# Performance work log

Measured on AMD Instinct MI355X. Metric: run time of the kernel, lower is better.

The kernel has to match this reference:

```python
import jax, jax.numpy as jnp
import numpy as np


def setup_inputs() -> dict:
    key = jax.random.key(0)
    ks = jax.random.split(key, 8)
    NUM_REL, D, E2, NUM_ENT = 500, 128, 3000000, 200000
    return {
        "rel_embed": jax.random.normal(ks[0], (NUM_REL, D), jnp.float32),
        "rel_embed_in": jax.random.normal(ks[1], (NUM_REL, D), jnp.float32),
        "rel_embed_out": jax.random.normal(ks[2], (NUM_REL, D), jnp.float32),
        "w_in": jax.random.normal(ks[3], (D, D), jnp.float32) * (D ** -0.5),
        "w_out": jax.random.normal(ks[4], (D, D), jnp.float32) * (D ** -0.5),
        "bn_gamma": jnp.ones((D,), jnp.float32),
        "bn_beta": jnp.zeros((D,), jnp.float32),
        "edge_index": jax.random.randint(ks[5], (2, E2), 0, NUM_ENT, jnp.int64 if jax.config.x64_enabled else jnp.int32),
        "edge_type": jax.random.randint(ks[6], (E2,), 0, NUM_REL, jnp.int64 if jax.config.x64_enabled else jnp.int32),
        "num_ent": NUM_ENT,
    }


def _edge_norm(edge_index, num_ent):
    # symmetric-normalization: deg^-1/2[row] * deg^-1/2[col]
    row, col = edge_index[0], edge_index[1]
    deg = jax.ops.segment_sum(jnp.ones(row.shape, jnp.float32), row, num_segments=num_ent)
    deg_inv = jnp.where(deg > 0, jax.lax.rsqrt(deg), 0.0)
    return deg_inv[row] * deg_inv[col]


def reference(rel_embed, rel_embed_in, rel_embed_out, w_in, w_out,
              bn_gamma, bn_beta, edge_index, edge_type, num_ent):
    E = edge_index.shape[1] // 2  # first half incoming, second half outgoing
    norm_in = _edge_norm(edge_index[:, :E], num_ent)    # [E]
    norm_out = _edge_norm(edge_index[:, E:], num_ent)   # [E]

    # gather relation embeds per edge, transform (per-edge matmul)
    neighs_in = rel_embed_in[edge_type[:E]] @ w_in      # [E, D]
    neighs_out = rel_embed_out[edge_type[E:]] @ w_out   # [E, D]

    # norm-weighted scatter-sum into entity buckets (rel_agg == 'sum')
    res_in = jax.ops.segment_sum(neighs_in * norm_in[:, None], edge_index[0, :E], num_segments=num_ent)
    res_out = jax.ops.segment_sum(neighs_out * norm_out[:, None], edge_index[0, E:], num_segments=num_ent)

    h = 0.5 * res_in + 0.5 * res_out                    # [num_ent, D]
    # BatchNorm1d (training mode: batch stats, biased variance, eps=1e-5)
    mean = jnp.mean(h, axis=0)
    var = jnp.mean(jnp.square(h - mean), axis=0)
    res = jnp.tanh((h - mean) * jax.lax.rsqrt(var + 1e-5) * bn_gamma + bn_beta)
    return (res, rel_embed)
```

## Files before the change

kernel.cpp:

```cpp
#include <hip/hip_runtime.h>

#define D 128
#define BUNROLL 8
#define RPB 128
#define CAP 2560
#define MAXK 2048
#define CHUNK4 8192
#define STILE 1024

__device__ __forceinline__ unsigned f2bf_rne(float x) {
    unsigned u = __float_as_uint(x);
    return (u + 0x7fffu + ((u >> 16) & 1u)) >> 16;
}

__global__ void transform2_bf_kernel(const float* __restrict__ Rin, const float* __restrict__ Win,
                                     const float* __restrict__ Rout, const float* __restrict__ Wout,
                                     unsigned short* __restrict__ T_bf, int nrel) {
    __shared__ float row[D];
    int b = blockIdx.x;
    bool second = (b >= nrel);
    const float* R = second ? Rout : Rin;
    const float* W = second ? Wout : Win;
    int r = second ? b - nrel : b;
    int t = threadIdx.x;
    row[t] = R[r * D + t];
    __syncthreads();
    float acc = 0.f;
#pragma unroll 8
    for (int k = 0; k < D; ++k) acc += row[k] * W[k * D + t];
    T_bf[(size_t)b * D + t] = (unsigned short)f2bf_rne(acc);
}

__global__ void transform2_kernel(const float* __restrict__ Rin, const float* __restrict__ Win,
                                  const float* __restrict__ Rout, const float* __restrict__ Wout,
                                  float* __restrict__ T_all, int nrel) {
    __shared__ float row[D];
    int b = blockIdx.x;
    bool second = (b >= nrel);
    const float* R = second ? Rout : Rin;
    const float* W = second ? Wout : Win;
    int r = second ? b - nrel : b;
    int t = threadIdx.x;
    row[t] = R[r * D + t];
    __syncthreads();
    float acc = 0.f;
#pragma unroll 8
    for (int k = 0; k < D; ++k) acc += row[k] * W[k * D + t];
    T_all[(size_t)b * D + t] = acc;
}

__global__ __launch_bounds__(512) void hist4_kernel(
        const int* __restrict__ rows, int E2,
        unsigned* __restrict__ cnt, int NB, int K) {
    __shared__ unsigned h[MAXK];
    int tid = threadIdx.x, blk = blockIdx.x;
    for (int i = tid; i < K; i += 512) h[i] = 0;
    __syncthreads();
    long s = (long)blk * CHUNK4;
    long e = s + CHUNK4; if (e > E2) e = E2;
    long n = e - s;
    if ((n & 3) == 0) {
        const int4* r4 = (const int4*)(rows + s);
        int m = (int)(n >> 2);
        for (int i = tid; i < m; i += 512) {
            int4 r = r4[i];
            atomicAdd(&h[((unsigned)r.x) >> 7], 1u);
            atomicAdd(&h[((unsigned)r.y) >> 7], 1u);
            atomicAdd(&h[((unsigned)r.z) >> 7], 1u);
            atomicAdd(&h[((unsigned)r.w) >> 7], 1u);
        }
    } else {
        for (long i = s + tid; i < e; i += 512)
            atomicAdd(&h[((unsigned)rows[i]) >> 7], 1u);
    }
    __syncthreads();
    for (int i = tid; i < K; i += 512)
        cnt[(size_t)i * NB + blk] = h[i];
}

__global__ __launch_bounds__(256) void tile_sum_u32(const unsigned int* __restrict__ cnt,
                                                    unsigned int* __restrict__ tsum, int n) {
    int tid = threadIdx.x;
    int i0 = blockIdx.x * STILE + tid * 4;
    unsigned int s = 0;
#pragma unroll
    for (int k = 0; k < 4; ++k) {
        int i = i0 + k;
        if (i < n) s += cnt[i];
    }
    __shared__ unsigned int ls[256];
    ls[tid] = s;
    __syncthreads();
    for (int off = 128; off >= 1; off >>= 1) {
        if (tid < off) ls[tid] += ls[tid + off];
        __syncthreads();
    }
    if (tid == 0) tsum[blockIdx.x] = ls[0];
}

__global__ void scan_tiles_kernel(const unsigned int* __restrict__ tile_sums,
                                  unsigned int* __restrict__ tile_off,
                                  unsigned int* __restrict__ base, int ntiles, int n) {
    int t = threadIdx.x;
    __shared__ unsigned int ls[1024];
    unsigned int v = (t < ntiles) ? tile_sums[t] : 0u;
    ls[t] = v;
    __syncthreads();
    for (int off = 1; off < 1024; off <<= 1) {
        unsigned int add = (t >= off) ? ls[t - off] : 0u;
        __syncthreads();
        ls[t] += add;
        __syncthreads();
    }
    if (t < ntiles) tile_off[t] = ls[t] - v;
    if (t == 1023) base[n] = ls[1023];
}

__global__ __launch_bounds__(256) void base_write_u32(const unsigned int* __restrict__ cnt,
                                                      const unsigned int* __restrict__ tile_off,
                                                      unsigned int* __restrict__ base, int n) {
    int tid = threadIdx.x;
    int i0 = blockIdx.x * STILE + tid * 4;
    unsigned int c[4];
#pragma unroll
    for (int k = 0; k < 4; ++k) {
        int i = i0 + k;
        c[k] = (i < n) ? cnt[i] : 0u;
    }
    unsigned int s = c[0] + c[1] + c[2] + c[3];
    __shared__ unsigned int ls[256];
    ls[tid] = s;
    __syncthreads();
    for (int off = 1; off < 256; off <<= 1) {
        unsigned int add = (tid >= off) ? ls[tid - off] : 0u;
        __syncthreads();
        ls[tid] += add;
        __syncthreads();
    }
    unsigned int run = (tid > 0 ? ls[tid - 1] : 0u) + tile_off[blockIdx.x];
#pragma unroll
    for (int k = 0; k < 4; ++k) {
        int i = i0 + k;
        if (i < n) base[i] = run;
        run += c[k];
    }
}

__global__ __launch_bounds__(512) void scatter4_kernel(
        const int* __restrict__ rows, const int* __restrict__ cols,
        const int* __restrict__ etype, const unsigned* __restrict__ base,
        uint2* __restrict__ payload, int E, int E2, int nrel, int NB, int K) {
    __shared__ unsigned cur[MAXK];
    int tid = threadIdx.x, blk = blockIdx.x;
    for (int i = tid; i < K; i += 512) cur[i] = base[(size_t)i * NB + blk];
    __syncthreads();
    long s = (long)blk * CHUNK4;
    long e = s + CHUNK4; if (e > E2) e = E2;
    long n = e - s;
    if ((n & 3) == 0) {
        const int4* r4 = (const int4*)(rows + s);
        const int4* c4 = (const int4*)(cols + s);
        const int4* t4 = (const int4*)(etype + s);
        int m = (int)(n >> 2);
        for (int i = tid; i < m; i += 512) {
            int4 r = r4[i];
            int4 c = c4[i];
            int4 t = t4[i];
            long e0 = s + ((long)i << 2);
            unsigned pos, ty;
            ty = (unsigned)t.x + ((e0 + 0 < E) ? 0u : (unsigned)nrel);
            pos = atomicAdd(&cur[((unsigned)r.x) >> 7], 1u);
            payload[pos] = make_uint2((unsigned)c.x, (((unsigned)r.x & 127u) << 10) | ty);
            ty = (unsigned)t.y + ((e0 + 1 < E) ? 0u : (unsigned)nrel);
            pos = atomicAdd(&cur[((unsigned)r.y) >> 7], 1u);
            payload[pos] = make_uint2((unsigned)c.y, (((unsigned)r.y & 127u) << 10) | ty);
            ty = (unsigned)t.z + ((e0 + 2 < E) ? 0u : (unsigned)nrel);
            pos = atomicAdd(&cur[((unsigned)r.z) >> 7], 1u);
            payload[pos] = make_uint2((unsigned)c.z, (((unsigned)r.z & 127u) << 10) | ty);
            ty = (unsigned)t.w + ((e0 + 3 < E) ? 0u : (unsigned)nrel);
            pos = atomicAdd(&cur[((unsigned)r.w) >> 7], 1u);
            payload[pos] = make_uint2((unsigned)c.w, (((unsigned)r.w & 127u) << 10) | ty);
        }
    } else {
        for (long i = s + tid; i < e; i += 512) {
            unsigned r = (unsigned)rows[i];
            unsigned c = (unsigned)cols[i];
            unsigned t = (unsigned)etype[i];
            unsigned ty = t + ((i < E) ? 0u : (unsigned)nrel);
            unsigned pos = atomicAdd(&cur[r >> 7], 1u);
            payload[pos] = make_uint2(c, ((r & 127u) << 10) | ty);
        }
    }
}

__global__ __launch_bounds__(512) void degsort_kernel(
        const unsigned* __restrict__ base, const uint2* __restrict__ payload,
        float* __restrict__ dinvAll, unsigned* __restrict__ rowBase,
        int nent, int nrel, int NB, int K) {
    __shared__ unsigned h2[RPB * 2];
    __shared__ unsigned sc[RPB];
    int tid = threadIdx.x, b = blockIdx.x;
    if (tid < RPB * 2) h2[tid] = 0;
    __syncthreads();
    size_t NBK = (size_t)NB * K;
    unsigned s = base[(size_t)b * NB];
    unsigned e = (b + 1 < K) ? base[(size_t)(b + 1) * NB] : base[NBK];
    for (unsigned i = s + tid; i < e; i += 512) {
        unsigned y = payload[i].y;
        unsigned lr = (y >> 10) & 127u;
        unsigned fo = ((y & 1023u) >= (unsigned)nrel) ? 1u : 0u;
        atomicAdd(&h2[lr * 2 + fo], 1u);
    }
    __syncthreads();
    unsigned tot = 0;
    if (tid < RPB) { tot = h2[tid * 2] + h2[tid * 2 + 1]; sc[tid] = tot; }
    __syncthreads();
    for (int off = 1; off < RPB; off <<= 1) {
        unsigned v = 0;
        if (tid < RPB && tid >= off) v = sc[tid - off];
        __syncthreads();
        if (tid < RPB) sc[tid] += v;
        __syncthreads();
    }
    if (tid < RPB) {
        rowBase[(size_t)b * RPB + tid] = sc[tid] - tot;
        int row = (b << 7) + tid;
        if (row < nent) {
            unsigned a = h2[tid * 2], o = h2[tid * 2 + 1];
            dinvAll[row]        = a ? rsqrtf((float)a) : 0.f;
            dinvAll[nent + row] = o ? rsqrtf((float)o) : 0.f;
        }
    }
}

__global__ __launch_bounds__(512) void accum4_kernel(
        const unsigned* __restrict__ base, const uint2* __restrict__ payload,
        const unsigned short* __restrict__ T_bf, const float* __restrict__ dinvAll,
        const unsigned* __restrict__ rowBase,
        float* __restrict__ out, float* __restrict__ sums, float* __restrict__ sumsq,
        int nent, int nrel, int NB, int K) {
    __shared__ uint2 sp[CAP];
    __shared__ unsigned hstart[RPB];
    __shared__ unsigned hcur[RPB];
    __shared__ float ls[D], lq[D];
    int tid = threadIdx.x;
    int b = blockIdx.x;
    size_t NBK = (size_t)NB * K;
    unsigned start = base[(size_t)b * NB];
    unsigned end   = (b + 1 < K) ? base[(size_t)(b + 1) * NB] : base[NBK];
    int n = (int)(end - start);
    int nin = n < CAP ? n : CAP;

    if (tid < RPB) { ls[tid] = 0.f; lq[tid] = 0.f; }

    if (n <= CAP) {
        if (tid < RPB) {
            unsigned v = rowBase[(size_t)b * RPB + tid];
            hstart[tid] = v;
            hcur[tid] = v;
        }
        __syncthreads();
        for (int i = tid; i < nin; i += 512) {
            uint2 p = payload[start + i];
            unsigned pos = atomicAdd(&hcur[(p.y >> 10) & 127u], 1u);
            sp[pos] = p;
        }
        __syncthreads();
    } else {
        if (tid < RPB) hstart[tid] = 0;
        __syncthreads();
        for (int i = tid; i < nin; i += 512)
            atomicAdd(&hstart[(payload[start + i].y >> 10) & 127u], 1u);
        __syncthreads();
        for (int off = 1; off < RPB; off <<= 1) {
            unsigned v = 0;
            if (tid < RPB && tid >= off) v = hstart[tid - off];
            __syncthreads();
            if (tid < RPB) hstart[tid] += v;
            __syncthreads();
        }
        unsigned ex = 0;
        if (tid < RPB) ex = tid ? hstart[tid - 1] : 0u;
        __syncthreads();
        if (tid < RPB) { hstart[tid] = ex; hcur[tid] = ex; }
        __syncthreads();
        for (int i = tid; i < nin; i += 512) {
            uint2 p = payload[start + i];
            unsigned pos = atomicAdd(&hcur[(p.y >> 10) & 127u], 1u);
            sp[pos] = p;
        }
        __syncthreads();
    }

    const uint2* T2 = (const uint2*)T_bf;
    float4* out4 = (float4*)out;
    int hw = tid >> 5, l32 = tid & 31;
    int row0 = b << 7;
    unsigned unrel = (unsigned)nrel;
    float4 s4 = make_float4(0.f, 0.f, 0.f, 0.f);
    float4 q4 = make_float4(0.f, 0.f, 0.f, 0.f);
    for (int rr = 0; rr < 8; ++rr) {
        int r = (hw << 3) + rr;
        int row = row0 + r;
        float da_in = 0.f, da_out = 0.f;
        if (row < nent) { da_in = dinvAll[row]; da_out = dinvAll[nent + row]; }
        unsigned s0 = hstart[r];
        unsigned s1 = (r < RPB - 1) ? hstart[r + 1] : (unsigned)nin;
        float4 a = make_float4(0.f, 0.f, 0.f, 0.f);
        unsigned i = s0;
        for (; i + 4 <= s1; i += 4) {
            uint2 p0 = sp[i], p1 = sp[i + 1], p2 = sp[i + 2], p3 = sp[i + 3];
            unsigned ty0 = p0.y & 1023u, ty1 = p1.y & 1023u;
            unsigned ty2 = p2.y & 1023u, ty3 = p3.y & 1023u;
            bool f0 = ty0 < unrel, f1 = ty1 < unrel, f2 = ty2 < unrel, f3 = ty3 < unrel;
            float dc0 = dinvAll[(f0 ? 0 : nent) + p0.x];
            float dc1 = dinvAll[(f1 ? 0 : nent) + p1.x];
            float dc2 = dinvAll[(f2 ? 0 : nent) + p2.x];
            float dc3 = dinvAll[(f3 ? 0 : nent) + p3.x];
            uint2 t0 = T2[(size_t)ty0 * 32 + l32];
            uint2 t1 = T2[(size_t)ty1 * 32 + l32];
            uint2 t2 = T2[(size_t)ty2 * 32 + l32];
            uint2 t3 = T2[(size_t)ty3 * 32 + l32];
            float c0 = 0.5f * (f0 ? da_in : da_out) * dc0;
            float c1 = 0.5f * (f1 ? da_in : da_out) * dc1;
            float c2 = 0.5f * (f2 ? da_in : da_out) * dc2;
            float c3 = 0.5f * (f3 ? da_in : da_out) * dc3;
            a.x += c0 * __uint_as_float(t0.x << 16);
            a.y += c0 * __uint_as_float(t0.x & 0xffff0000u);
            a.z += c0 * __uint_as_float(t0.y << 16);
            a.w += c0 * __uint_as_float(t0.y & 0xffff0000u);
            a.x += c1 * __uint_as_float(t1.x << 16);
            a.y += c1 * __uint_as_float(t1.x & 0xffff0000u);
            a.z += c1 * __uint_as_float(t1.y << 16);
            a.w += c1 * __uint_as_float(t1.y & 0xffff0000u);
            a.x += c2 * __uint_as_float(t2.x << 16);
            a.y += c2 * __uint_as_float(t2.x & 0xffff0000u);
            a.z += c2 * __uint_as_float(t2.y << 16);
            a.w += c2 * __uint_as_float(t2.y & 0xffff0000u);
            a.x += c3 * __uint_as_float(t3.x << 16);
            a.y += c3 * __uint_as_float(t3.x & 0xffff0000u);
            a.z += c3 * __uint_as_float(t3.y << 16);
            a.w += c3 * __uint_as_float(t3.y & 0xffff0000u);
        }
        for (; i < s1; ++i) {
            uint2 p = sp[i];
            unsigned ty = p.y & 1023u;
            bool f = ty < unrel;
            float c = 0.5f * (f ? da_in : da_out) * dinvAll[(f ? 0 : nent) + p.x];
            uint2 t = T2[(size_t)ty * 32 + l32];
            a.x += c * __uint_as_float(t.x << 16);
            a.y += c * __uint_as_float(t.x & 0xffff0000u);
            a.z += c * __uint_as_float(t.y << 16);
            a.w += c * __uint_as_float(t.y & 0xffff0000u);
        }
        for (unsigned j = start + (unsigned)nin; j < end; ++j) {
            uint2 p = payload[j];
            if (((p.y >> 10) & 127u) == (unsigned)r) {
                unsigned ty = p.y & 1023u;
                bool f = ty < unrel;
                float c = 0.5f * (f ? da_in : da_out) * dinvAll[(f ? 0 : nent) + p.x];
                uint2 t = T2[(size_t)ty * 32 + l32];
                a.x += c * __uint_as_float(t.x << 16);
                a.y += c * __uint_as_float(t.x & 0xffff0000u);
                a.z += c * __uint_as_float(t.y << 16);
                a.w += c * __uint_as_float(t.y & 0xffff0000u);
            }
        }
        if (row < nent) {
            out4[(size_t)row * 32 + l32] = a;
            s4.x += a.x; s4.y += a.y; s4.z += a.z; s4.w += a.w;
            q4.x += a.x * a.x; q4.y += a.y * a.y; q4.z += a.z * a.z; q4.w += a.w * a.w;
        }
    }
    atomicAdd(&ls[4 * l32 + 0], s4.x); atomicAdd(&ls[4 * l32 + 1], s4.y);
    atomicAdd(&ls[4 * l32 + 2], s4.z); atomicAdd(&ls[4 * l32 + 3], s4.w);
    atomicAdd(&lq[4 * l32 + 0], q4.x); atomicAdd(&lq[4 * l32 + 1], q4.y);
    atomicAdd(&lq[4 * l32 + 2], q4.z); atomicAdd(&lq[4 * l32 + 3], q4.w);
    __syncthreads();
    if (tid < D) {
        atomicAdd(&sums[tid], ls[tid]);
        atomicAdd(&sumsq[tid], lq[tid]);
    }
}

__global__ void bn_coef_kernel(const float* __restrict__ sums, const float* __restrict__ sumsq,
                               const float* __restrict__ gamma, const float* __restrict__ beta,
                               float* __restrict__ scale, float* __restrict__ shift, int nent) {
    int c = threadIdx.x;
    float inv_n = 1.0f / (float)nent;
    float mean = sums[c] * inv_n;
    float var = sumsq[c] * inv_n - mean * mean;
    float istd = rsqrtf(var + 1e-5f);
    float sc = istd * gamma[c];
    scale[c] = sc;
    shift[c] = beta[c] - mean * sc;
}

__global__ __launch_bounds__(256) void bn_apply2_kernel(
        float* __restrict__ h, const float* __restrict__ scale, const float* __restrict__ shift,
        const float* __restrict__ rel_embed, float* __restrict__ pass, int nent, int npass4) {
    __shared__ float s_sc[D], s_sh[D];
    if (threadIdx.x < D) { s_sc[threadIdx.x] = scale[threadIdx.x]; s_sh[threadIdx.x] = shift[threadIdx.x]; }
    __syncthreads();
    long total = (long)nent * (D / 4);
    long stride = (long)gridDim.x * blockDim.x;
    long idx0 = (long)blockIdx.x * blockDim.x + threadIdx.x;
    float4* h4 = (float4*)h;
    for (long i = idx0; i < total; i += stride) {
        int c0 = (int)((i & 31) << 2);
        float4 v = h4[i];
        v.x = tanhf(v.x * s_sc[c0 + 0] + s_sh[c0 + 0]);
        v.y = tanhf(v.y * s_sc[c0 + 1] + s_sh[c0 + 1]);
        v.z = tanhf(v.z * s_sc[c0 + 2] + s_sh[c0 + 2]);
        v.w = tanhf(v.w * s_sc[c0 + 3] + s_sh[c0 + 3]);
        h4[i] = v;
    }
    const float4* re4 = (const float4*)rel_embed;
    float4* p4 = (float4*)pass;
    for (long i = idx0; i < npass4; i += stride) p4[i] = re4[i];
}

__global__ __launch_bounds__(256) void degree_kernel(const int* __restrict__ rows, int E,
                                                     float* __restrict__ deg_in,
                                                     float* __restrict__ deg_out) {
    int total = 2 * E;
    int tid = blockIdx.x * blockDim.x + threadIdx.x;
    int nth = gridDim.x * blockDim.x;
    for (long b = (long)tid * BUNROLL; b < total; b += (long)nth * BUNROLL) {
        for (int k = 0; k < BUNROLL && b + k < total; ++k) {
            int r = rows[b + k];
            float* deg = (b + k < E) ? deg_in : deg_out;
            atomicAdd(&deg[r], 1.0f);
        }
    }
}

__global__ void scatter_kernel(const int* __restrict__ rows, const int* __restrict__ cols,
                               const int* __restrict__ etype,
                               const float* __restrict__ deg_in, const float* __restrict__ deg_out,
                               const float* __restrict__ T_in, const float* __restrict__ T_out,
                               float* __restrict__ out, int E) {
    int wave = (blockIdx.x * blockDim.x + threadIdx.x) >> 6;
    int lane = threadIdx.x & 63;
    int nwaves = (gridDim.x * blockDim.x) >> 6;
    int total = 2 * E;
    for (int e = wave; e < total; e += nwaves) {
        bool first = (e < E);
        int row = rows[e];
        int col = cols[e];
        int t = etype[e];
        const float* deg = first ? deg_in : deg_out;
        const float* T = first ? T_in : T_out;
        float dr = deg[row];
        float dc = deg[col];
        float norm = (dr > 0.f ? rsqrtf(dr) : 0.f) * (dc > 0.f ? rsqrtf(dc) : 0.f);
        float c = 0.5f * norm;
        if (c != 0.f) {
            float v0 = c * T[t * D + lane];
            float v1 = c * T[t * D + 64 + lane];
            long b = (long)row * D;
            atomicAdd(&out[b + lane], v0);
            atomicAdd(&out[b + 64 + lane], v1);
        }
    }
}

__global__ void bn_stats_kernel(const float* __restrict__ h, int nent,
                                float* __restrict__ sums, float* __restrict__ sumsq) {
    int col = threadIdx.x;
    float s = 0.f, s2 = 0.f;
    for (int r = blockIdx.x; r < nent; r += gridDim.x) {
        float v = h[(long)r * D + col];
        s += v;
        s2 += v * v;
    }
    atomicAdd(&sums[col], s);
    atomicAdd(&sumsq[col], s2);
}

__global__ void bn_apply_kernel(float* __restrict__ h,
                                const float* __restrict__ sums, const float* __restrict__ sumsq,
                                const float* __restrict__ gamma, const float* __restrict__ beta,
                                int nent) {
    long total = ((long)nent * D) / 4;
    long stride = (long)gridDim.x * blockDim.x;
    float inv_n = 1.0f / (float)nent;
    float4* h4 = (float4*)h;
    for (long i = (long)blockIdx.x * blockDim.x + threadIdx.x; i < total; i += stride) {
        int c0 = (int)((i * 4) & (D - 1));
        float4 v = h4[i];
        float r[4] = {v.x, v.y, v.z, v.w};
#pragma unroll
        for (int j = 0; j < 4; ++j) {
            int col = c0 + j;
            float mean = sums[col] * inv_n;
            float var = sumsq[col] * inv_n - mean * mean;
            float istd = rsqrtf(var + 1e-5f);
            r[j] = tanhf((r[j] - mean) * istd * gamma[col] + beta[col]);
        }
        h4[i] = make_float4(r[0], r[1], r[2], r[3]);
    }
}

extern "C" void kernel_launch(void* const* d_in, const int* in_sizes, int n_in,
                              void* d_out, int out_size, void* d_ws, size_t ws_size,
                              hipStream_t stream) {
    const float* rel_embed     = (const float*)d_in[0];
    const float* rel_embed_in  = (const float*)d_in[1];
    const float* rel_embed_out = (const float*)d_in[2];
    const float* w_in          = (const float*)d_in[3];
    const float* w_out         = (const float*)d_in[4];
    const float* bn_gamma      = (const float*)d_in[5];
    const float* bn_beta       = (const float*)d_in[6];
    const int*   edge_index    = (const int*)d_in[7];
    const int*   edge_type     = (const int*)d_in[8];

    const int nrel = in_sizes[0] / D;
    const int E2   = in_sizes[8];
    const int E    = E2 / 2;
    const int nent = (out_size - in_sizes[0]) / D;
    const int K    = (nent + RPB - 1) / RPB;
    const int NB   = (E2 + CHUNK4 - 1) / CHUNK4;
    const long NBK = (long)NB * K;
    const int ntiles = (int)((NBK + STILE - 1) / STILE);

    float* out = (float*)d_out;
    const int* rows = edge_index;
    const int* cols = edge_index + E2;

    float*          ws       = (float*)d_ws;
    float*          dinvAll  = ws;
    float*          sums     = dinvAll + (size_t)2 * nent;
    float*          sumsq    = sums + D;
    float*          scale    = sumsq + D;
    float*          shift    = scale + D;
    unsigned*       rowBase  = (unsigned*)(shift + D);
    unsigned*       cnt      = rowBase + (size_t)K * RPB;
    unsigned*       tsum     = cnt + NBK + 1;
    unsigned*       toff     = tsum + ntiles;
    unsigned short* T_bf     = (unsigned short*)(toff + ntiles);
    uintptr_t pal = ((uintptr_t)(T_bf + (size_t)2 * nrel * D) + 15) & ~(uintptr_t)15;
    uint2*          payload  = (uint2*)pal;
    size_t needed = (pal + (size_t)E2 * sizeof(uint2)) - (uintptr_t)d_ws;

    bool fast = (needed <= ws_size) && (K <= MAXK) && (2 * nrel <= 1024) &&
                (ntiles <= 1024);

    if (fast) {
        hipMemsetAsync(sums, 0, (size_t)2 * D * sizeof(float), stream);

        transform2_bf_kernel<<<2 * nrel, D, 0, stream>>>(rel_embed_in, w_in,
                                                         rel_embed_out, w_out, T_bf, nrel);
        hist4_kernel<<<NB, 512, 0, stream>>>(rows, E2, cnt, NB, K);
        tile_sum_u32<<<ntiles, 256, 0, stream>>>(cnt, tsum, (int)NBK);
        scan_tiles_kernel<<<1, 1024, 0, stream>>>(tsum, toff, cnt, ntiles, (int)NBK);
        base_write_u32<<<ntiles, 256, 0, stream>>>(cnt, toff, cnt, (int)NBK);
        scatter4_kernel<<<NB, 512, 0, stream>>>(rows, cols, edge_type, cnt,
                                                payload, E, E2, nrel, NB, K);
        degsort_kernel<<<K, 512, 0, stream>>>(cnt, payload, dinvAll, rowBase,
                                              nent, nrel, NB, K);
        accum4_kernel<<<K, 512, 0, stream>>>(cnt, payload, T_bf, dinvAll, rowBase,
                                             out, sums, sumsq, nent, nrel, NB, K);
        bn_coef_kernel<<<1, D, 0, stream>>>(sums, sumsq, bn_gamma, bn_beta,
                                            scale, shift, nent);
        bn_apply2_kernel<<<2048, 256, 0, stream>>>(out, scale, shift, rel_embed,
                                                   out + (size_t)nent * D, nent,
                                                   (nrel * D) / 4);
    } else {
        float* f_deg_in  = ws;
        float* f_deg_out = f_deg_in + nent;
        float* f_T_in    = f_deg_out + nent;
        float* f_T_out   = f_T_in + (size_t)nrel * D;
        float* f_sums    = f_T_out + (size_t)nrel * D;
        float* f_sumsq   = f_sums + D;

        hipMemsetAsync(out, 0, (size_t)nent * D * sizeof(float), stream);
        hipMemsetAsync(f_deg_in, 0, (size_t)2 * nent * sizeof(float), stream);
        hipMemsetAsync(f_sums, 0, (size_t)2 * D * sizeof(float), stream);

        transform2_kernel<<<2 * nrel, D, 0, stream>>>(rel_embed_in, w_in, rel_embed_out, w_out,
                                                      f_T_in, nrel);
        degree_kernel<<<1466, 256, 0, stream>>>(edge_index, E, f_deg_in, f_deg_out);
        scatter_kernel<<<2048, 256, 0, stream>>>(rows, cols, edge_type, f_deg_in, f_deg_out,
                                                 f_T_in, f_T_out, out, E);
        bn_stats_kernel<<<1024, D, 0, stream>>>(out, nent, f_sums, f_sumsq);
        bn_apply_kernel<<<4096, 256, 0, stream>>>(out, f_sums, f_sumsq, bn_gamma, bn_beta, nent);
        hipMemcpyAsync(out + (size_t)nent * D, rel_embed,
                       (size_t)nrel * D * sizeof(float), hipMemcpyDeviceToDevice, stream);
    }
}
```

Baseline: 227.2 us.

## Store pre-BN activations as bf16 and interleave two rows per warp in accumulation

The accumulation kernel now processes two destination rows at once, interleaving their edge loops to raise memory-level parallelism. It also writes the intermediate h in bf16 to a workspace buffer instead of fp32 into the output, and the BN apply kernel reads that buffer. This halves intermediate write and read traffic (about 100MB down to 50MB each way). The cost is that bf16 rounding of h, applied before normalization, adds precision error. BN statistics are still computed in fp32.

```diff
diff --git a/kernel.cpp b/kernel.cpp
--- a/kernel.cpp
+++ b/kernel.cpp
@@ -12,6 +12,12 @@
     unsigned u = __float_as_uint(x);
     return (u + 0x7fffu + ((u >> 16) & 1u)) >> 16;
 }
+
+#define FMA4(a, c, t)                                        \
+    (a).x += (c) * __uint_as_float((t).x << 16);             \
+    (a).y += (c) * __uint_as_float((t).x & 0xffff0000u);     \
+    (a).z += (c) * __uint_as_float((t).y << 16);             \
+    (a).w += (c) * __uint_as_float((t).y & 0xffff0000u);
 
 __global__ void transform2_bf_kernel(const float* __restrict__ Rin, const float* __restrict__ Win,
                                      const float* __restrict__ Rout, const float* __restrict__ Wout,
@@ -233,11 +239,42 @@
     }
 }
 
+#define DRAIN4(i, s1, a, dain, daout)                                            \
+    for (; (i) + 4 <= (s1); (i) += 4) {                                          \
+        uint2 p0 = sp[(i)], p1 = sp[(i) + 1], p2 = sp[(i) + 2], p3 = sp[(i) + 3];\
+        unsigned ty0 = p0.y & 1023u, ty1 = p1.y & 1023u;                         \
+        unsigned ty2 = p2.y & 1023u, ty3 = p3.y & 1023u;                         \
+        bool f0 = ty0 < unrel, f1 = ty1 < unrel;                                 \
+        bool f2 = ty2 < unrel, f3 = ty3 < unrel;                                 \
+        float dc0 = dinvAll[(f0 ? 0 : nent) + p0.x];                             \
+        float dc1 = dinvAll[(f1 ? 0 : nent) + p1.x];                             \
+        float dc2 = dinvAll[(f2 ? 0 : nent) + p2.x];                             \
+        float dc3 = dinvAll[(f3 ? 0 : nent) + p3.x];                             \
+        uint2 t0 = T2[(size_t)ty0 * 32 + l32];                                   \
+        uint2 t1 = T2[(size_t)ty1 * 32 + l32];                                   \
+        uint2 t2 = T2[(size_t)ty2 * 32 + l32];                                   \
+        uint2 t3 = T2[(size_t)ty3 * 32 + l32];                                   \
+        float c0 = 0.5f * (f0 ? (dain) : (daout)) * dc0;                         \
+        float c1 = 0.5f * (f1 ? (dain) : (daout)) * dc1;                         \
+        float c2 = 0.5f * (f2 ? (dain) : (daout)) * dc2;                         \
+        float c3 = 0.5f * (f3 ? (dain) : (daout)) * dc3;                         \
+        FMA4(a, c0, t0) FMA4(a, c1, t1) FMA4(a, c2, t2) FMA4(a, c3, t3)          \
+    }                                                                            \
+    for (; (i) < (s1); ++(i)) {                                                  \
+        uint2 p = sp[(i)];                                                       \
+        unsigned ty = p.y & 1023u;                                               \
+        bool f = ty < unrel;                                                     \
+        float c = 0.5f * (f ? (dain) : (daout)) * dinvAll[(f ? 0 : nent) + p.x]; \
+        uint2 t = T2[(size_t)ty * 32 + l32];                                     \
+        FMA4(a, c, t)                                                            \
+    }
+
 __global__ __launch_bounds__(512) void accum4_kernel(
         const unsigned* __restrict__ base, const uint2* __restrict__ payload,
         const unsigned short* __restrict__ T_bf, const float* __restrict__ dinvAll,
         const unsigned* __restrict__ rowBase,
-        float* __restrict__ out, float* __restrict__ sums, float* __restrict__ sumsq,
+        float* __restrict__ out, unsigned short* __restrict__ h_bf, int use_bf,
+        float* __restrict__ sums, float* __restrict__ sumsq,
         int nent, int nrel, int NB, int K) {
     __shared__ uint2 sp[CAP];
     __shared__ unsigned hstart[RPB];
@@ -294,82 +331,95 @@
 
     const uint2* T2 = (const uint2*)T_bf;
     float4* out4 = (float4*)out;
+    uint2* hb2 = (uint2*)h_bf;
     int hw = tid >> 5, l32 = tid & 31;
     int row0 = b << 7;
     unsigned unrel = (unsigned)nrel;
     float4 s4 = make_float4(0.f, 0.f, 0.f, 0.f);
     float4 q4 = make_float4(0.f, 0.f, 0.f, 0.f);
-    for (int rr = 0; rr < 8; ++rr) {
-        int r = (hw << 3) + rr;
-        int row = row0 + r;
-        float da_in = 0.f, da_out = 0.f;
-        if (row < nent) { da_in = dinvAll[row]; da_out = dinvAll[nent + row]; }
-        unsigned s0 = hstart[r];
-        unsigned s1 = (r < RPB - 1) ? hstart[r + 1] : (unsigned)nin;
-        float4 a = make_float4(0.f, 0.f, 0.f, 0.f);
-        unsigned i = s0;
-        for (; i + 4 <= s1; i += 4) {
-            uint2 p0 = sp[i], p1 = sp[i + 1], p2 = sp[i + 2], p3 = sp[i + 3];
-            unsigned ty0 = p0.y & 1023u, ty1 = p1.y & 1023u;
-            unsigned ty2 = p2.y & 1023u, ty3 = p3.y & 1023u;
-            bool f0 = ty0 < unrel, f1 = ty1 < unrel, f2 = ty2 < unrel, f3 = ty3 < unrel;
-            float dc0 = dinvAll[(f0 ? 0 : nent) + p0.x];
-            float dc1 = dinvAll[(f1 ? 0 : nent) + p1.x];
-            float dc2 = dinvAll[(f2 ? 0 : nent) + p2.x];
-            float dc3 = dinvAll[(f3 ? 0 : nent) + p3.x];
-            uint2 t0 = T2[(size_t)ty0 * 32 + l32];
-            uint2 t1 = T2[(size_t)ty1 * 32 + l32];
-            uint2 t2 = T2[(size_t)ty2 * 32 + l32];
-            uint2 t3 = T2[(size_t)ty3 * 32 + l32];
-            float c0 = 0.5f * (f0 ? da_in : da_out) * dc0;
-            float c1 = 0.5f * (f1 ? da_in : da_out) * dc1;
-            float c2 = 0.5f * (f2 ? da_in : da_out) * dc2;
-            float c3 = 0.5f * (f3 ? da_in : da_out) * dc3;
-            a.x += c0 * __uint_as_float(t0.x << 16);
-            a.y += c0 * __uint_as_float(t0.x & 0xffff0000u);
-            a.z += c0 * __uint_as_float(t0.y << 16);
-            a.w += c0 * __uint_as_float(t0.y & 0xffff0000u);
-            a.x += c1 * __uint_as_float(t1.x << 16);
-            a.y += c1 * __uint_as_float(t1.x & 0xffff0000u);
-            a.z += c1 * __uint_as_float(t1.y << 16);
-            a.w += c1 * __uint_as_float(t1.y & 0xffff0000u);
-            a.x += c2 * __uint_as_float(t2.x << 16);
-            a.y += c2 * __uint_as_float(t2.x & 0xffff0000u);
-            a.z += c2 * __uint_as_float(t2.y << 16);
-            a.w += c2 * __uint_as_float(t2.y & 0xffff0000u);
-            a.x += c3 * __uint_as_float(t3.x << 16);
-            a.y += c3 * __uint_as_float(t3.x & 0xffff0000u);
-            a.z += c3 * __uint_as_float(t3.y << 16);
-            a.w += c3 * __uint_as_float(t3.y & 0xffff0000u);
-        }
-        for (; i < s1; ++i) {
-            uint2 p = sp[i];
-            unsigned ty = p.y & 1023u;
-            bool f = ty < unrel;
-            float c = 0.5f * (f ? da_in : da_out) * dinvAll[(f ? 0 : nent) + p.x];
-            uint2 t = T2[(size_t)ty * 32 + l32];
-            a.x += c * __uint_as_float(t.x << 16);
-            a.y += c * __uint_as_float(t.x & 0xffff0000u);
-            a.z += c * __uint_as_float(t.y << 16);
-            a.w += c * __uint_as_float(t.y & 0xffff0000u);
-        }
-        for (unsigned j = start + (unsigned)nin; j < end; ++j) {
-            uint2 p = payload[j];
-            if (((p.y >> 10) & 127u) == (unsigned)r) {
-                unsigned ty = p.y & 1023u;
-                bool f = ty < unrel;
-                float c = 0.5f * (f ? da_in : da_out) * dinvAll[(f ? 0 : nent) + p.x];
-                uint2 t = T2[(size_t)ty * 32 + l32];
-                a.x += c * __uint_as_float(t.x << 16);
-                a.y += c * __uint_as_float(t.x & 0xffff0000u);
-                a.z += c * __uint_as_float(t.y << 16);
-                a.w += c * __uint_as_float(t.y & 0xffff0000u);
+
+    for (int rp = 0; rp < 4; ++rp) {
+        int rA = (hw << 3) + rp * 2;
+        int rB = rA + 1;
+        int rowA = row0 + rA, rowB = row0 + rB;
+        float daA_in = 0.f, daA_out = 0.f, daB_in = 0.f, daB_out = 0.f;
+        if (rowA < nent) { daA_in = dinvAll[rowA]; daA_out = dinvAll[nent + rowA]; }
+        if (rowB < nent) { daB_in = dinvAll[rowB]; daB_out = dinvAll[nent + rowB]; }
+        unsigned sA1 = hstart[rA + 1];
+        unsigned sB1 = (rB < RPB - 1) ? hstart[rB + 1] : (unsigned)nin;
+        unsigned iA = hstart[rA], iB = sA1;
+        float4 aA = make_float4(0.f, 0.f, 0.f, 0.f);
+        float4 aB = make_float4(0.f, 0.f, 0.f, 0.f);
+
+        while (iA + 2 <= sA1 && iB + 2 <= sB1) {
+            uint2 pA0 = sp[iA], pA1 = sp[iA + 1];
+            uint2 pB0 = sp[iB], pB1 = sp[iB + 1];
+            unsigned tyA0 = pA0.y & 1023u, tyA1 = pA1.y & 1023u;
+            unsigned tyB0 = pB0.y & 1023u, tyB1 = pB1.y & 1023u;
+            bool fA0 = tyA0 < unrel, fA1 = tyA1 < unrel;
+            bool fB0 = tyB0 < unrel, fB1 = tyB1 < unrel;
+            float dcA0 = dinvAll[(fA0 ? 0 : nent) + pA0.x];
+            float dcA1 = dinvAll[(fA1 ? 0 : nent) + pA1.x];
+            float dcB0 = dinvAll[(fB0 ? 0 : nent) + pB0.x];
+            float dcB1 = dinvAll[(fB1 ? 0 : nent) + pB1.x];
+            uint2 tA0 = T2[(size_t)tyA0 * 32 + l32];
+            uint2 tA1 = T2[(size_t)tyA1 * 32 + l32];
+            uint2 tB0 = T2[(size_t)tyB0 * 32 + l32];
+            uint2 tB1 = T2[(size_t)tyB1 * 32 + l32];
+            float cA0 = 0.5f * (fA0 ? daA_in : daA_out) * dcA0;
+            float cA1 = 0.5f * (fA1 ? daA_in : daA_out) * dcA1;
+            float cB0 = 0.5f * (fB0 ? daB_in : daB_out) * dcB0;
+            float cB1 = 0.5f * (fB1 ? daB_in : daB_out) * dcB1;
+            FMA4(aA, cA0, tA0) FMA4(aA, cA1, tA1)
+            FMA4(aB, cB0, tB0) FMA4(aB, cB1, tB1)
+            iA += 2; iB += 2;
+        }
+        DRAIN4(iA, sA1, aA, daA_in, daA_out)
+        DRAIN4(iB, sB1, aB, daB_in, daB_out)
+
+        if (n > CAP) {
+            for (unsigned j2 = start + (unsigned)nin; j2 < end; ++j2) {
+                uint2 p = payload[j2];
+                unsigned lr = (p.y >> 10) & 127u;
+                if (lr == (unsigned)rA || lr == (unsigned)rB) {
+                    unsigned ty = p.y & 1023u;
+                    bool f = ty < unrel;
+                    float dc = dinvAll[(f ? 0 : nent) + p.x];
+                    uint2 t = T2[(size_t)ty * 32 + l32];
+                    if (lr == (unsigned)rA) {
+                        float c = 0.5f * (f ? daA_in : daA_out) * dc;
+                        FMA4(aA, c, t)
+                    } else {
+                        float c = 0.5f * (f ? daB_in : daB_out) * dc;
+                        FMA4(aB, c, t)
+                    }
+                }
             }
         }
-        if (row < nent) {
-            out4[(size_t)row * 32 + l32] = a;
-            s4.x += a.x; s4.y += a.y; s4.z += a.z; s4.w += a.w;
-            q4.x += a.x * a.x; q4.y += a.y * a.y; q4.z += a.z * a.z; q4.w += a.w * a.w;
+
+        if (rowA < nent) {
+            if (use_bf) {
+                hb2[(size_t)rowA * 32 + l32] = make_uint2(
+                    f2bf_rne(aA.x) | (f2bf_rne(aA.y) << 16),
+                    f2bf_rne(aA.z) | (f2bf_rne(aA.w) << 16));
+            } else {
+                out4[(size_t)rowA * 32 + l32] = aA;
+            }
+            s4.x += aA.x; s4.y += aA.y; s4.z += aA.z; s4.w += aA.w;
+            q4.x += aA.x * aA.x; q4.y += aA.y * aA.y;
+            q4.z += aA.z * aA.z; q4.w += aA.w * aA.w;
+        }
+        if (rowB < nent) {
+            if (use_bf) {
+                hb2[(size_t)rowB * 32 + l32] = make_uint2(
+                    f2bf_rne(aB.x) | (f2bf_rne(aB.y) << 16),
+                    f2bf_rne(aB.z) | (f2bf_rne(aB.w) << 16));
+            } else {
+                out4[(size_t)rowB * 32 + l32] = aB;
+            }
+            s4.x += aB.x; s4.y += aB.y; s4.z += aB.z; s4.w += aB.w;
+            q4.x += aB.x * aB.x; q4.y += aB.y * aB.y;
+            q4.z += aB.z * aB.z; q4.w += aB.w * aB.w;
         }
     }
     atomicAdd(&ls[4 * l32 + 0], s4.x); atomicAdd(&ls[4 * l32 + 1], s4.y);
@@ -394,6 +444,33 @@
     float sc = istd * gamma[c];
     scale[c] = sc;
     shift[c] = beta[c] - mean * sc;
+}
+
+__global__ __launch_bounds__(256) void bn_apply2_bf_kernel(
+        const unsigned short* __restrict__ h_bf, float* __restrict__ out,
+        const float* __restrict__ scale, const float* __restrict__ shift,
+        const float* __restrict__ rel_embed, float* __restrict__ pass, int nent, int npass4) {
+    __shared__ float s_sc[D], s_sh[D];
+    if (threadIdx.x < D) { s_sc[threadIdx.x] = scale[threadIdx.x]; s_sh[threadIdx.x] = shift[threadIdx.x]; }
+    __syncthreads();
+    long total = (long)nent * 32;
+    long stride = (long)gridDim.x * blockDim.x;
+    long idx0 = (long)blockIdx.x * blockDim.x + threadIdx.x;
+    const uint2* hb2 = (const uint2*)h_bf;
+    float4* out4 = (float4*)out;
+    for (long i = idx0; i < total; i += stride) {
+        int c0 = (int)((i & 31) << 2);
+        uint2 v = hb2[i];
+        float4 o;
+        o.x = tanhf(__uint_as_float(v.x << 16)         * s_sc[c0 + 0] + s_sh[c0 + 0]);
+        o.y = tanhf(__uint_as_float(v.x & 0xffff0000u) * s_sc[c0 + 1] + s_sh[c0 + 1]);
+        o.z = tanhf(__uint_as_float(v.y << 16)         * s_sc[c0 + 2] + s_sh[c0 + 2]);
+        o.w = tanhf(__uint_as_float(v.y & 0xffff0000u) * s_sc[c0 + 3] + s_sh[c0 + 3]);
+        out4[i] = o;
+    }
+    const float4* re4 = (const float4*)rel_embed;
+    float4* p4 = (float4*)pass;
+    for (long i = idx0; i < npass4; i += stride) p4[i] = re4[i];
 }
 
 __global__ __launch_bounds__(256) void bn_apply2_kernel(
@@ -541,10 +618,14 @@
     unsigned short* T_bf     = (unsigned short*)(toff + ntiles);
     uintptr_t pal = ((uintptr_t)(T_bf + (size_t)2 * nrel * D) + 15) & ~(uintptr_t)15;
     uint2*          payload  = (uint2*)pal;
-    size_t needed = (pal + (size_t)E2 * sizeof(uint2)) - (uintptr_t)d_ws;
-
-    bool fast = (needed <= ws_size) && (K <= MAXK) && (2 * nrel <= 1024) &&
-                (ntiles <= 1024);
+    uintptr_t pal2 = ((uintptr_t)(payload + E2) + 15) & ~(uintptr_t)15;
+    unsigned short* h_bf     = (unsigned short*)pal2;
+    size_t needed    = pal2 - (uintptr_t)d_ws;
+    size_t needed_bf = needed + (size_t)nent * D * sizeof(unsigned short);
+
+    bool fast   = (needed <= ws_size) && (K <= MAXK) && (2 * nrel <= 1024) &&
+                  (ntiles <= 1024);
+    int  use_bf = fast && (needed_bf <= ws_size);
 
     if (fast) {
         hipMemsetAsync(sums, 0, (size_t)2 * D * sizeof(float), stream);
@@ -560,12 +641,19 @@
         degsort_kernel<<<K, 512, 0, stream>>>(cnt, payload, dinvAll, rowBase,
                                               nent, nrel, NB, K);
         accum4_kernel<<<K, 512, 0, stream>>>(cnt, payload, T_bf, dinvAll, rowBase,
-                                             out, sums, sumsq, nent, nrel, NB, K);
+                                             out, h_bf, use_bf, sums, sumsq,
+                                             nent, nrel, NB, K);
         bn_coef_kernel<<<1, D, 0, stream>>>(sums, sumsq, bn_gamma, bn_beta,
                                             scale, shift, nent);
-        bn_apply2_kernel<<<2048, 256, 0, stream>>>(out, scale, shift, rel_embed,
-                                                   out + (size_t)nent * D, nent,
-                                                   (nrel * D) / 4);
+        if (use_bf) {
+            bn_apply2_bf_kernel<<<2048, 256, 0, stream>>>(h_bf, out, scale, shift, rel_embed,
+                                                          out + (size_t)nent * D, nent,
+                                                          (nrel * D) / 4);
+        } else {
+            bn_apply2_kernel<<<2048, 256, 0, stream>>>(out, scale, shift, rel_embed,
+                                                       out + (size_t)nent * D, nent,
+                                                       (nrel * D) / 4);
+        }
     } else {
         float* f_deg_in  = ws;
         float* f_deg_out = f_deg_in + nent;
```

Result: no change. 225.6 us (-0.7%).
